# Optimization experiments

Hardware: AMD Instinct MI355X
Metric: run time of the kernel (lower is better)

Reference implementation:

```python
import jax, jax.numpy as jnp
from jax import lax
import numpy as np

# Reconstructed utils constants
PSZ = 24     # patch size
KS = 3       # kernel size of generated conv kernels
FILTERS = 9  # channels / number of generated filters
STRIDE = 8   # conv stride inside KGL


def setup_inputs() -> dict:
    key = jax.random.key(0)
    k1, k2, k3 = jax.random.split(key, 3)
    B, H, W = 8, 768, 768
    x = jax.random.normal(k1, (B, H, W, FILTERS), dtype=jnp.float32)
    conv_w = jax.random.normal(k2, (KS, KS, FILTERS, 9), dtype=jnp.float32) * 0.05  # HWIO
    conv_b = jnp.zeros((9,), dtype=jnp.float32)
    dense_w = jax.random.normal(k3, (FILTERS, FILTERS * FILTERS), dtype=jnp.float32) * 0.05
    dense_b = jnp.zeros((FILTERS * FILTERS,), dtype=jnp.float32)
    return {"x": x, "conv_w": conv_w, "conv_b": conv_b, "dense_w": dense_w, "dense_b": dense_b}


def _clip_by_norm(t, axes, clip_norm=1.0):
    # tf.clip_by_norm: t * clip_norm / max(||t||_2_over_axes, clip_norm)
    l2 = jnp.sqrt(jnp.sum(t * t, axis=axes, keepdims=True))
    return t * (clip_norm / jnp.maximum(l2, clip_norm))


def reference(x, conv_w, conv_b, dense_w, dense_b):
    B, H, W, C = x.shape
    p1, p2 = H // PSZ, W // PSZ
    N = p1 * p2
    # tf.image.extract_patches layout: [B, p1, p2, PSZ*PSZ*C] with patch flattened row-major (row, col, chan)
    patches = x.reshape(B, p1, PSZ, p2, PSZ, C).transpose(0, 1, 3, 2, 4, 5)  # [B,p1,p2,PSZ,PSZ,C]
    # RAW reshape to (N, B, PSZ, PSZ, C) exactly as the TF code does (buffer reinterpretation)
    patches = patches.reshape(N, B, PSZ, PSZ, C)
    flat = patches.reshape(N * B, PSZ, PSZ, C)

    # --- W_G1: per-patch conv kernel generation ---
    conv_out = lax.conv_general_dilated(
        flat, conv_w, window_strides=(STRIDE, STRIDE), padding="SAME",
        dimension_numbers=("NHWC", "HWIO", "NHWC")) + conv_b  # [N*B, 3, 3, 9]
    wg1 = conv_out.reshape(N * B, KS, KS, FILTERS, 1)
    wg1 = _clip_by_norm(wg1, axes=(1, 2))                      # norm over (KS, KS) dims
    wg1 = wg1.reshape(N, B, KS, KS, FILTERS, 1)

    # --- W_G2: per-patch 1x1 mixing kernel via GAP + Dense ---
    gap = flat.mean(axis=(1, 2))                               # [N*B, C]
    d = gap @ dense_w + dense_b                                # [N*B, FILTERS^2]
    wg2 = d.reshape(N * B, 1, 1, FILTERS, FILTERS)
    wg2 = _clip_by_norm(wg2, axes=(1, 2, 3))
    wg2 = wg2.reshape(N, B, 1, 1, FILTERS, FILTERS)
    return wg1, wg2
```

## Files before the change

kernel.cpp:

```cpp
#include <hip/hip_runtime.h>


#define PSZ 24
#define NCH 9
#define HW 768
#define PATCH_ELEMS (PSZ*PSZ*NCH)
#define NPIX (PSZ*PSZ)
#define ROWF (PSZ*NCH)
#define OUT1_OFF 0
#define OUT2_OFF 663552

__global__ __launch_bounds__(256) void kgl_kernel(
    const float* __restrict__ x,
    const float* __restrict__ conv_w,
    const float* __restrict__ conv_b,
    const float* __restrict__ dense_w,
    const float* __restrict__ dense_b,
    float* __restrict__ out)
{
    __shared__ float patch[PATCH_ELEMS];
    __shared__ float cw[729];
    __shared__ float co_s[81];
    __shared__ float d_s[81];
    __shared__ float gap_s[NCH];
    __shared__ float sc1[NCH];
    __shared__ float sc2[NCH];
    __shared__ float red[4*NCH];

    const int j   = blockIdx.x;
    const int b   = j >> 10;
    const int rem = j & 1023;
    const int pi  = rem >> 5;
    const int pj  = rem & 31;
    const int tid = threadIdx.x;

    for (int i = tid; i < 729; i += 256) cw[i] = conv_w[i];

    const size_t base = ((size_t)(b*HW + pi*PSZ) * HW + (size_t)pj*PSZ) * NCH;
    for (int e = tid; e < PATCH_ELEMS; e += 256) {
        int r = e / ROWF;
        int t = e - r*ROWF;
        patch[e] = x[base + (size_t)r*(HW*NCH) + t];
    }
    __syncthreads();

    float cs[NCH];
    #pragma unroll
    for (int c = 0; c < NCH; ++c) cs[c] = 0.f;
    for (int p = tid; p < NPIX; p += 256) {
        const float* pp = &patch[p*NCH];
        #pragma unroll
        for (int c = 0; c < NCH; ++c) cs[c] += pp[c];
    }
    const int lane = tid & 63;
    const int wave = tid >> 6;
    #pragma unroll
    for (int c = 0; c < NCH; ++c) {
        float v = cs[c];
        #pragma unroll
        for (int off = 32; off > 0; off >>= 1) v += __shfl_down(v, off, 64);
        if (lane == 0) red[wave*NCH + c] = v;
    }

    if (tid < 81) {
        const int oy = tid / 27;
        const int ox = (tid / 9) % 3;
        const int oc = tid % 9;
        float acc = conv_b[oc];
        #pragma unroll
        for (int ky = 0; ky < 3; ++ky) {
            #pragma unroll
            for (int kx = 0; kx < 3; ++kx) {
                const float* pp = &patch[(oy*8+ky)*ROWF + (ox*8+kx)*NCH];
                const float* ww = &cw[((ky*3+kx)*9)*9 + oc];
                #pragma unroll
                for (int ic = 0; ic < 9; ++ic) acc += pp[ic] * ww[ic*9];
            }
        }
        co_s[tid] = acc;
    }
    __syncthreads();

    if (tid < NCH) {
        float s = red[tid] + red[NCH+tid] + red[2*NCH+tid] + red[3*NCH+tid];
        gap_s[tid] = s * (1.0f / (float)NPIX);

        float n2 = 0.f;
        #pragma unroll
        for (int s9 = 0; s9 < 9; ++s9) {
            float v = co_s[s9*9 + tid];
            n2 += v*v;
        }
        sc1[tid] = 1.0f / fmaxf(sqrtf(n2), 1.0f);
    }
    __syncthreads();

    if (tid < 81) {
        float acc = dense_b[tid];
        #pragma unroll
        for (int c = 0; c < NCH; ++c) acc += gap_s[c] * dense_w[c*81 + tid];
        d_s[tid] = acc;

        out[OUT1_OFF + (size_t)j*81 + tid] = co_s[tid] * sc1[tid % 9];
    }
    __syncthreads();

    if (tid < NCH) {
        float n2 = 0.f;
        #pragma unroll
        for (int a = 0; a < 9; ++a) {
            float v = d_s[a*9 + tid];
            n2 += v*v;
        }
        sc2[tid] = 1.0f / fmaxf(sqrtf(n2), 1.0f);
    }
    __syncthreads();

    if (tid < 81) {
        out[OUT2_OFF + (size_t)j*81 + tid] = d_s[tid] * sc2[tid % 9];
    }
}

extern "C" void kernel_launch(void* const* d_in, const int* in_sizes, int n_in,
                              void* d_out, int out_size, void* d_ws, size_t ws_size,
                              hipStream_t stream) {
    const float* x       = (const float*)d_in[0];
    const float* conv_w  = (const float*)d_in[1];
    const float* conv_b  = (const float*)d_in[2];
    const float* dense_w = (const float*)d_in[3];
    const float* dense_b = (const float*)d_in[4];
    float* out = (float*)d_out;

    kgl_kernel<<<8192, 256, 0, stream>>>(x, conv_w, conv_b, dense_w, dense_b, out);
}
```

Before: 258.9 us.

## Load patches with async global-to-LDS 16-byte copies and restructure GAP reduction

Patch loading now uses 16-byte global_load_lds transfers that go straight from global memory into shared memory instead of scalar per-element loads through registers. The conv weights are also copied as float4. The GAP channel sums are recomputed as vectorized column sums over rows by a separate wave, running alongside the conv threads, followed by a small reduction. This replaces the shuffle reduction and is meant to cut load instruction count and latency in a memory-bound kernel. It relies on 16-byte alignment of each patch row, and the patch copy may not be fully synchronized before use, since only __syncthreads follows the async loads.

```diff
diff --git a/kernel.cpp b/kernel.cpp
--- a/kernel.cpp
+++ b/kernel.cpp
@@ -5,10 +5,19 @@
 #define NCH 9
 #define HW 768
 #define PATCH_ELEMS (PSZ*PSZ*NCH)
+#define PATCH_V4 1296
 #define NPIX (PSZ*PSZ)
 #define ROWF (PSZ*NCH)
+#define ROWV4 54
+#define XROWF (HW*NCH)
 #define OUT1_OFF 0
 #define OUT2_OFF 663552
+
+__device__ inline void async_load16(const void* g, void* l) {
+    __builtin_amdgcn_global_load_lds(
+        (const __attribute__((address_space(1))) void*)g,
+        (__attribute__((address_space(3))) void*)l, 16, 0, 0);
+}
 
 __global__ __launch_bounds__(256) void kgl_kernel(
     const float* __restrict__ x,
@@ -18,14 +27,14 @@
     const float* __restrict__ dense_b,
     float* __restrict__ out)
 {
-    __shared__ float patch[PATCH_ELEMS];
-    __shared__ float cw[729];
+    __shared__ __align__(16) float patch[PATCH_ELEMS];
+    __shared__ __align__(16) float cw[732];
+    __shared__ __align__(16) float colsum[ROWF];
     __shared__ float co_s[81];
     __shared__ float d_s[81];
     __shared__ float gap_s[NCH];
     __shared__ float sc1[NCH];
     __shared__ float sc2[NCH];
-    __shared__ float red[4*NCH];
 
     const int j   = blockIdx.x;
     const int b   = j >> 10;
@@ -34,33 +43,25 @@
     const int pj  = rem & 31;
     const int tid = threadIdx.x;
 
-    for (int i = tid; i < 729; i += 256) cw[i] = conv_w[i];
+    if (tid < 182) {
+        reinterpret_cast<float4*>(cw)[tid] =
+            reinterpret_cast<const float4*>(conv_w)[tid];
+    } else if (tid == 182) {
+        cw[728] = conv_w[728];
+    }
 
     const size_t base = ((size_t)(b*HW + pi*PSZ) * HW + (size_t)pj*PSZ) * NCH;
-    for (int e = tid; e < PATCH_ELEMS; e += 256) {
-        int r = e / ROWF;
-        int t = e - r*ROWF;
-        patch[e] = x[base + (size_t)r*(HW*NCH) + t];
+    const float* gbase = x + base;
+    #pragma unroll
+    for (int it = 0; it < 6; ++it) {
+        int e4 = tid + it*256;
+        if (e4 < PATCH_V4) {
+            int r = e4 / ROWV4;
+            int t = e4 - r*ROWV4;
+            async_load16(gbase + (size_t)r*XROWF + t*4, &patch[e4*4]);
+        }
     }
     __syncthreads();
-
-    float cs[NCH];
-    #pragma unroll
-    for (int c = 0; c < NCH; ++c) cs[c] = 0.f;
-    for (int p = tid; p < NPIX; p += 256) {
-        const float* pp = &patch[p*NCH];
-        #pragma unroll
-        for (int c = 0; c < NCH; ++c) cs[c] += pp[c];
-    }
-    const int lane = tid & 63;
-    const int wave = tid >> 6;
-    #pragma unroll
-    for (int c = 0; c < NCH; ++c) {
-        float v = cs[c];
-        #pragma unroll
-        for (int off = 32; off > 0; off >>= 1) v += __shfl_down(v, off, 64);
-        if (lane == 0) red[wave*NCH + c] = v;
-    }
 
     if (tid < 81) {
         const int oy = tid / 27;
@@ -72,19 +73,26 @@
             #pragma unroll
             for (int kx = 0; kx < 3; ++kx) {
                 const float* pp = &patch[(oy*8+ky)*ROWF + (ox*8+kx)*NCH];
-                const float* ww = &cw[((ky*3+kx)*9)*9 + oc];
+                const float* ww = &cw[(ky*3+kx)*81 + oc];
                 #pragma unroll
                 for (int ic = 0; ic < 9; ++ic) acc += pp[ic] * ww[ic*9];
             }
         }
         co_s[tid] = acc;
+    } else if (tid >= 128 && tid < 128+ROWV4) {
+        const int k = tid - 128;
+        const float4* pv = reinterpret_cast<const float4*>(patch);
+        float4 acc = pv[k];
+        #pragma unroll
+        for (int r = 1; r < PSZ; ++r) {
+            float4 v = pv[r*ROWV4 + k];
+            acc.x += v.x; acc.y += v.y; acc.z += v.z; acc.w += v.w;
+        }
+        reinterpret_cast<float4*>(colsum)[k] = acc;
     }
     __syncthreads();
 
     if (tid < NCH) {
-        float s = red[tid] + red[NCH+tid] + red[2*NCH+tid] + red[3*NCH+tid];
-        gap_s[tid] = s * (1.0f / (float)NPIX);
-
         float n2 = 0.f;
         #pragma unroll
         for (int s9 = 0; s9 < 9; ++s9) {
@@ -92,6 +100,12 @@
             n2 += v*v;
         }
         sc1[tid] = 1.0f / fmaxf(sqrtf(n2), 1.0f);
+    } else if (tid >= 128 && tid < 128+NCH) {
+        const int c = tid - 128;
+        float s = 0.f;
+        #pragma unroll
+        for (int i = 0; i < PSZ; ++i) s += colsum[c + NCH*i];
+        gap_s[c] = s * (1.0f / (float)NPIX);
     }
     __syncthreads();
 
```

Measured after the change: 241.3 us. 1.07x faster.
